# Performance work log

Measured on AMD Instinct MI355X. Metric: run time of the kernel, lower is better.

Reference implementation:

```python
import jax, jax.numpy as jnp
import numpy as np

SLOPE = 0.1
HEADS = 4
BN_EPS = 1e-5


def _gat(x, W, a_src, a_dst, mask):
    # x: (B,N,D); W: (D,D); a_src/a_dst: (H,dh); mask: (B,N,N) bool
    B, N, D = x.shape
    dh = D // HEADS
    h = (x @ W).reshape(B, N, HEADS, dh)
    s_src = jnp.einsum('bnhd,hd->bhn', h, a_src)  # score contrib of query i
    s_dst = jnp.einsum('bnhd,hd->bhn', h, a_dst)  # score contrib of key j
    e = jax.nn.leaky_relu(s_src[:, :, :, None] + s_dst[:, :, None, :], SLOPE)  # (B,H,N,N)
    e = jnp.where(mask[:, None, :, :], e, jnp.float32(-1e9))
    a = jax.nn.softmax(e, axis=-1)
    out = jnp.einsum('bhij,bjhd->bihd', a, h).reshape(B, N, D)
    return out


def setup_inputs() -> dict:
    key = jax.random.key(0)
    ks = jax.random.split(key, 20)
    B, N, F, D, Hn = 2, 2000, 64, 128, 3
    deep_dim = 3 * D
    feats = jax.random.normal(ks[0], (B, N, F), dtype=jnp.float32)
    ind = jax.random.randint(ks[1], (B, N, N), 0, 2).astype(bool)
    eye = jnp.eye(N, dtype=bool)[None]
    ind = jnp.logical_or(ind, eye)  # ensure self-loops so no all-masked row
    uni = jnp.ones((B, N, N), dtype=bool)
    s = 0.05
    return {
        'features': feats,
        'industry_mask': ind,
        'universe_mask': uni,
        # BatchNorm1d (eval mode)
        'bn_gamma': jax.random.normal(ks[2], (F,)) * s + 1.0,
        'bn_beta': jax.random.normal(ks[3], (F,)) * s,
        'bn_mean': jnp.zeros((F,), jnp.float32),
        'bn_var': jnp.ones((F,), jnp.float32),
        # encoder MLP (stored as (in,out))
        'W1': jax.random.normal(ks[4], (F, D)) * s,
        'b1': jnp.zeros((D,), jnp.float32),
        'W2': jax.random.normal(ks[5], (D, D)) * s,
        'b2': jnp.zeros((D,), jnp.float32),
        # industry GAT
        'giW': jax.random.normal(ks[6], (D, D)) * s,
        'gia_src': jax.random.normal(ks[7], (HEADS, D // HEADS)) * s,
        'gia_dst': jax.random.normal(ks[8], (HEADS, D // HEADS)) * s,
        # universe GAT
        'guW': jax.random.normal(ks[9], (D, D)) * s,
        'gua_src': jax.random.normal(ks[10], (HEADS, D // HEADS)) * s,
        'gua_dst': jax.random.normal(ks[11], (HEADS, D // HEADS)) * s,
        # per-horizon deep factor heads (Hn, deep_dim), (Hn,)
        'head_W': jax.random.normal(ks[12], (Hn, deep_dim)) * s,
        'head_b': jnp.zeros((Hn,), jnp.float32),
        # per-horizon factor attention proj (Hn, F, F), applied as x @ P_h^T
        'proj_W': jax.random.normal(ks[13], (Hn, F, F)) * s,
    }


def reference(features, industry_mask, universe_mask, bn_gamma, bn_beta, bn_mean,
              bn_var, W1, b1, W2, b2, giW, gia_src, gia_dst, guW, gua_src,
              gua_dst, head_W, head_b, proj_W):
    # --- StockContextEncoder: BN (eval) + MLP ---
    xn = (features - bn_mean) * jax.lax.rsqrt(bn_var + BN_EPS) * bn_gamma + bn_beta
    C = jax.nn.relu(xn @ W1 + b1) @ W2 + b2  # (B,N,D)
    # --- masked GATs with residual subtraction ---
    H_I = _gat(C, giW, gia_src, gia_dst, industry_mask)
    C_bar_I = C - H_I
    H_U = _gat(C_bar_I, guW, gua_src, gua_dst, universe_mask)
    C_bar_U = C_bar_I - H_U
    concat_ctx = jnp.concatenate([C, C_bar_I, C_bar_U], axis=-1)  # (B,N,3D)
    # --- per-horizon deep factor heads (vectorized over horizons) ---
    factors = jax.nn.leaky_relu(
        jnp.einsum('bnd,hd->hbn', concat_ctx, head_W) + head_b[:, None, None], SLOPE)
    # --- FactorAttention (Eq. 9-12), vectorized over horizons ---
    U = jax.nn.leaky_relu(jnp.einsum('bnm,hkm->hbnk', features, proj_W), SLOPE)
    A = jax.nn.softmax(U, axis=-1)          # (Hn,B,N,m)
    a_bar = A.mean(axis=2)                  # (Hn,B,m)
    recon = jnp.einsum('bnm,hbm->hbn', features, a_bar)
    return (C, C_bar_I, C_bar_U, H_I, H_U, factors, recon, A)
```

## Files before the change

### kernel.cpp

```cpp
#include <hip/hip_runtime.h>

#define BB 2
#define NN 2000
#define FF 64
#define DD 128
#define NH 4
#define HNZ 3
#define DEEP 384
#define NSEG 8
#define SEGSTRIDE 256
#define HTPAD 2048

typedef __attribute__((ext_vector_type(8))) short short8;
typedef __attribute__((ext_vector_type(4))) float f32x4;
typedef unsigned short ushort_t;

__device__ __forceinline__ float lrelu(float x) { return x > 0.f ? x : 0.1f * x; }
__device__ __forceinline__ ushort_t f2bf(float f) {
    unsigned int u = __float_as_uint(f);
    unsigned int r = u + 0x7fffu + ((u >> 16) & 1u);
    return (ushort_t)(r >> 16);
}

__global__ __launch_bounds__(128) void k_enc_proj(
    const float* __restrict__ feat, const float* __restrict__ gamma,
    const float* __restrict__ beta, const float* __restrict__ mean,
    const float* __restrict__ var, const float* __restrict__ W1,
    const float* __restrict__ b1, const float* __restrict__ W2,
    const float* __restrict__ b2, float* __restrict__ C,
    const float* __restrict__ Wg, const float* __restrict__ a_src,
    const float* __restrict__ a_dst, ushort_t* __restrict__ hb_rm,
    float* __restrict__ ssrc, float* __restrict__ sdst)
{
    __shared__ float xnl[4][FF];
    __shared__ float hidl[4][DD];
    __shared__ float Cl[4][DD];
    const int row0 = blockIdx.x * 4;
    const int t = threadIdx.x;
    for (int idx = t; idx < 4 * FF; idx += 128) {
        int r = idx >> 6, m = idx & 63;
        float f = feat[(row0 + r) * FF + m];
        xnl[r][m] = (f - mean[m]) * rsqrtf(var[m] + 1e-5f) * gamma[m] + beta[m];
    }
    __syncthreads();
    float acc[4];
    const int j = t;
#pragma unroll
    for (int r = 0; r < 4; ++r) acc[r] = b1[j];
    for (int m = 0; m < FF; ++m) {
        float w = W1[m * DD + j];
#pragma unroll
        for (int r = 0; r < 4; ++r) acc[r] += xnl[r][m] * w;
    }
#pragma unroll
    for (int r = 0; r < 4; ++r) hidl[r][j] = fmaxf(acc[r], 0.f);
    __syncthreads();
#pragma unroll
    for (int r = 0; r < 4; ++r) acc[r] = b2[j];
    for (int k = 0; k < DD; ++k) {
        float w = W2[k * DD + j];
#pragma unroll
        for (int r = 0; r < 4; ++r) acc[r] += hidl[r][k] * w;
    }
#pragma unroll
    for (int r = 0; r < 4; ++r) {
        C[(row0 + r) * DD + j] = acc[r];
        Cl[r][j] = acc[r];
    }
    __syncthreads();
    float pacc[4] = {0.f, 0.f, 0.f, 0.f};
    for (int k = 0; k < DD; ++k) {
        float w = Wg[k * DD + j];
#pragma unroll
        for (int r = 0; r < 4; ++r) pacc[r] += Cl[r][k] * w;
    }
    const float as = a_src[j], ad = a_dst[j];
    const int head = j >> 5;
#pragma unroll
    for (int r = 0; r < 4; ++r) {
        hb_rm[(row0 + r) * DD + j] = f2bf(pacc[r]);
        float ps = pacc[r] * as;
        float pd = pacc[r] * ad;
#pragma unroll
        for (int off = 16; off; off >>= 1) {
            ps += __shfl_xor(ps, off, 32);
            pd += __shfl_xor(pd, off, 32);
        }
        if ((j & 31) == 0) {
            int row = row0 + r;
            int b = row / NN, n = row % NN;
            ssrc[(b * NH + head) * NN + n] = ps;
            sdst[(b * NH + head) * NN + n] = pd;
        }
    }
}

__global__ __launch_bounds__(128) void k_finish_proj(
    const float* __restrict__ C, const float* __restrict__ den,
    float* __restrict__ H, float* __restrict__ Cbar,
    const float* __restrict__ Wg, const float* __restrict__ a_src,
    const float* __restrict__ a_dst, ushort_t* __restrict__ hb_rm,
    float* __restrict__ ssrc, float* __restrict__ sdst)
{
    __shared__ float Xl[4][DD];
    const int row0 = blockIdx.x * 4;
    const int t = threadIdx.x;
    const int hh = t >> 5;
#pragma unroll
    for (int r = 0; r < 4; ++r) {
        int idx = (row0 + r) * DD + t;
        float dv = den[(row0 + r) * NH + hh];
        float Hv = H[idx] / dv;
        float cb = C[idx] - Hv;
        H[idx] = Hv;
        Cbar[idx] = cb;
        Xl[r][t] = cb;
    }
    __syncthreads();
    float pacc[4] = {0.f, 0.f, 0.f, 0.f};
    const int j = t;
    for (int k = 0; k < DD; ++k) {
        float w = Wg[k * DD + j];
#pragma unroll
        for (int r = 0; r < 4; ++r) pacc[r] += Xl[r][k] * w;
    }
    const float as = a_src[j], ad = a_dst[j];
    const int head = j >> 5;
#pragma unroll
    for (int r = 0; r < 4; ++r) {
        hb_rm[(row0 + r) * DD + j] = f2bf(pacc[r]);
        float ps = pacc[r] * as;
        float pd = pacc[r] * ad;
#pragma unroll
        for (int off = 16; off; off >>= 1) {
            ps += __shfl_xor(ps, off, 32);
            pd += __shfl_xor(pd, off, 32);
        }
        if ((j & 31) == 0) {
            int row = row0 + r;
            int b = row / NN, n = row % NN;
            ssrc[(b * NH + head) * NN + n] = ps;
            sdst[(b * NH + head) * NN + n] = pd;
        }
    }
}

__global__ __launch_bounds__(256) void k_transpose(
    const ushort_t* __restrict__ hb_rm, ushort_t* __restrict__ hT)
{
    __shared__ ushort_t tile[64][65];
    const int nblk = blockIdx.x & 31;
    const int dblk = (blockIdx.x >> 5) & 1;
    const int b = blockIdx.x >> 6;
    const int n0 = nblk * 64, d0 = dblk * 64;
    const int t = threadIdx.x;
#pragma unroll
    for (int e = 0; e < 16; ++e) {
        int lin = e * 256 + t;
        int n = lin >> 6, d = lin & 63;
        if (n0 + n < NN)
            tile[n][d] = hb_rm[(b * NN + n0 + n) * DD + d0 + d];
    }
    __syncthreads();
#pragma unroll
    for (int e = 0; e < 16; ++e) {
        int lin = e * 256 + t;
        int d = lin >> 6, n = lin & 63;
        if (n0 + n < NN)
            hT[(b * DD + d0 + d) * HTPAD + n0 + n] = tile[n][d];
    }
}

__global__ __launch_bounds__(256) void k_gat_attn(
    const int* __restrict__ mask, const ushort_t* __restrict__ hT,
    const float* __restrict__ ssrc, const float* __restrict__ sdst,
    float* __restrict__ Hnum, float* __restrict__ den_out)
{
    __shared__ float sdl[NH][SEGSTRIDE];
    const int t = threadIdx.x;
    const int iblk = blockIdx.x % 125;
    const int tmp = blockIdx.x / 125;
    const int b = tmp & 1;
    const int seg = tmp >> 1;
    const int i0 = iblk * 16;
    const int jbeg = seg * SEGSTRIDE;
    const int jlim = min(NN - jbeg, SEGSTRIDE);

    const int h = t >> 6;
    const int l = t & 63;
    const int il = l & 15;
    const int g = l >> 4;

    for (int jj = l; jj < jlim; jj += 64)
        sdl[h][jj] = sdst[(b * NH + h) * NN + jbeg + jj];
    __syncthreads();

    const float sS = ssrc[(b * NH + h) * NN + i0 + il];
    const int* mrow = mask + (long)b * NN * NN + (long)(i0 + il) * NN + jbeg;
    const ushort_t* hrow0 = hT + ((b * DD + 32 * h + il) * HTPAD + jbeg);
    const ushort_t* hrow1 = hrow0 + 16 * HTPAD;

    f32x4 acc0 = {0.f, 0.f, 0.f, 0.f};
    f32x4 acc1 = {0.f, 0.f, 0.f, 0.f};
    float den_acc = 0.f;

    for (int jc = 0; jc < SEGSTRIDE; jc += 32) {
        const int jloc = jc + 8 * g;
        int4 m0 = make_int4(0, 0, 0, 0), m1 = make_int4(0, 0, 0, 0);
        if (jloc < jlim)     m0 = *(const int4*)(mrow + jloc);
        if (jloc + 4 < jlim) m1 = *(const int4*)(mrow + jloc + 4);
        float4 s0 = *(const float4*)&sdl[h][jloc];
        float4 s1 = *(const float4*)&sdl[h][jloc + 4];
        float w[8];
        w[0] = m0.x ? __expf(lrelu(sS + s0.x)) : 0.f;
        w[1] = m0.y ? __expf(lrelu(sS + s0.y)) : 0.f;
        w[2] = m0.z ? __expf(lrelu(sS + s0.z)) : 0.f;
        w[3] = m0.w ? __expf(lrelu(sS + s0.w)) : 0.f;
        w[4] = m1.x ? __expf(lrelu(sS + s1.x)) : 0.f;
        w[5] = m1.y ? __expf(lrelu(sS + s1.y)) : 0.f;
        w[6] = m1.z ? __expf(lrelu(sS + s1.z)) : 0.f;
        w[7] = m1.w ? __expf(lrelu(sS + s1.w)) : 0.f;
        short8 af;
#pragma unroll
        for (int e = 0; e < 8; ++e) {
            den_acc += w[e];
            af[e] = (short)f2bf(w[e]);
        }
        short8 bf0 = *(const short8*)(hrow0 + jloc);
        short8 bf1 = *(const short8*)(hrow1 + jloc);
        acc0 = __builtin_amdgcn_mfma_f32_16x16x32_bf16(af, bf0, acc0, 0, 0, 0);
        acc1 = __builtin_amdgcn_mfma_f32_16x16x32_bf16(af, bf1, acc1, 0, 0, 0);
    }

    den_acc += __shfl_xor(den_acc, 16);
    den_acc += __shfl_xor(den_acc, 32);
    if (l < 16)
        atomicAdd(&den_out[(b * NN + i0 + l) * NH + h], den_acc);

#pragma unroll
    for (int r = 0; r < 4; ++r) {
        float* dst = &Hnum[((long)b * NN + i0 + 4 * g + r) * DD + 32 * h + il];
        atomicAdd(dst, acc0[r]);
        atomicAdd(dst + 16, acc1[r]);
    }
}

__global__ __launch_bounds__(256) void k_finish(
    const float* __restrict__ X, const float* __restrict__ den,
    float* __restrict__ H, float* __restrict__ Cbar)
{
    int idx = blockIdx.x * 256 + threadIdx.x;
    if (idx >= BB * NN * DD / 4) return;
    int row = idx >> 5;
    int d4 = idx & 31;
    float inv = 1.f / den[row * NH + (d4 >> 3)];
    float4 s = ((const float4*)H)[idx];
    float4 xv = ((const float4*)X)[idx];
    float4 ho = make_float4(s.x * inv, s.y * inv, s.z * inv, s.w * inv);
    ((float4*)H)[idx] = ho;
    ((float4*)Cbar)[idx] =
        make_float4(xv.x - ho.x, xv.y - ho.y, xv.z - ho.z, xv.w - ho.w);
}

__global__ __launch_bounds__(256) void k_factors(
    const float* __restrict__ C, const float* __restrict__ CbI,
    const float* __restrict__ CbU, const float* __restrict__ head_W,
    const float* __restrict__ head_b, float* __restrict__ factors)
{
    int out = blockIdx.x * 4 + (threadIdx.x >> 6);
    int l = threadIdx.x & 63;
    if (out >= HNZ * BB * NN) return;
    int h = out / (BB * NN);
    int rn = out % (BB * NN);
    const float* w = head_W + h * DEEP;
    float acc = C[rn * DD + l] * w[l] + C[rn * DD + l + 64] * w[l + 64]
              + CbI[rn * DD + l] * w[128 + l] + CbI[rn * DD + l + 64] * w[192 + l]
              + CbU[rn * DD + l] * w[256 + l] + CbU[rn * DD + l + 64] * w[320 + l];
#pragma unroll
    for (int off = 32; off; off >>= 1) acc += __shfl_xor(acc, off, 64);
    if (l == 0) factors[out] = lrelu(acc + head_b[h]);
}

__global__ __launch_bounds__(256) void k_factor_attn(
    const float* __restrict__ feat, const float* __restrict__ proj_W,
    float* __restrict__ A, float* __restrict__ abar)
{
    __shared__ float Pt[FF][FF + 1];
    __shared__ float fl[4][FF];
    __shared__ float abpart[4][FF];
    const int hb = blockIdx.x / 50;
    const int n_base = (blockIdx.x % 50) * 40;
    const int h = hb / BB, b = hb % BB;
    const int t = threadIdx.x;
    for (int idx = t; idx < FF * FF; idx += 256) {
        int k = idx >> 6, m = idx & 63;
        Pt[m][k] = proj_W[(h * FF + k) * FF + m];
    }
    const int ns = t >> 6, k = t & 63;
    float abp = 0.f;
    for (int cch = 0; cch < 10; ++cch) {
        int n0 = n_base + cch * 4;
        __syncthreads();
        for (int idx = t; idx < 4 * FF; idx += 256) {
            int r = idx >> 6, m = idx & 63;
            fl[r][m] = feat[(b * NN + n0 + r) * FF + m];
        }
        __syncthreads();
        float u = 0.f;
        for (int m = 0; m < FF; ++m) u += fl[ns][m] * Pt[m][k];
        u = lrelu(u);
        float mx = u;
#pragma unroll
        for (int off = 32; off; off >>= 1) mx = fmaxf(mx, __shfl_xor(mx, off, 64));
        float e = __expf(u - mx);
        float sm = e;
#pragma unroll
        for (int off = 32; off; off >>= 1) sm += __shfl_xor(sm, off, 64);
        float a = e / sm;
        A[((h * BB + b) * NN + n0 + ns) * FF + k] = a;
        abp += a;
    }
    abpart[ns][k] = abp;
    __syncthreads();
    if (t < FF) {
        float s = abpart[0][t] + abpart[1][t] + abpart[2][t] + abpart[3][t];
        atomicAdd(&abar[(h * BB + b) * FF + t], s);
    }
}

__global__ __launch_bounds__(256) void k_recon(
    const float* __restrict__ feat, const float* __restrict__ abar,
    float* __restrict__ recon)
{
    int out = blockIdx.x * 4 + (threadIdx.x >> 6);
    int l = threadIdx.x & 63;
    if (out >= HNZ * BB * NN) return;
    int h = out / (BB * NN);
    int rn = out % (BB * NN);
    float acc = feat[rn * FF + l] * abar[(h * BB + rn / NN) * FF + l];
#pragma unroll
    for (int off = 32; off; off >>= 1) acc += __shfl_xor(acc, off, 64);
    if (l == 0) recon[out] = acc * (1.f / NN);
}

extern "C" void kernel_launch(void* const* d_in, const int* in_sizes, int n_in,
                              void* d_out, int out_size, void* d_ws, size_t ws_size,
                              hipStream_t stream)
{
    const float* feat     = (const float*)d_in[0];
    const int*   ind_mask = (const int*)d_in[1];
    const int*   uni_mask = (const int*)d_in[2];
    const float* bn_gamma = (const float*)d_in[3];
    const float* bn_beta  = (const float*)d_in[4];
    const float* bn_mean  = (const float*)d_in[5];
    const float* bn_var   = (const float*)d_in[6];
    const float* W1 = (const float*)d_in[7];
    const float* b1 = (const float*)d_in[8];
    const float* W2 = (const float*)d_in[9];
    const float* b2 = (const float*)d_in[10];
    const float* giW = (const float*)d_in[11];
    const float* gia_src = (const float*)d_in[12];
    const float* gia_dst = (const float*)d_in[13];
    const float* guW = (const float*)d_in[14];
    const float* gua_src = (const float*)d_in[15];
    const float* gua_dst = (const float*)d_in[16];
    const float* head_W = (const float*)d_in[17];
    const float* head_b = (const float*)d_in[18];
    const float* proj_W = (const float*)d_in[19];

    float* out = (float*)d_out;
    float* C       = out;
    float* CbI     = out + 512000;
    float* CbU     = out + 1024000;
    float* H_I     = out + 1536000;
    float* H_U     = out + 2048000;
    float* factors = out + 2560000;
    float* recon   = out + 2572000;
    float* A       = out + 2584000;

    float* ws = (float*)d_ws;
    ushort_t* hb_rm = (ushort_t*)ws;
    ushort_t* hT    = (ushort_t*)(ws + 256000);
    float* ssrc = ws + 518144;
    float* sdst = ws + 534144;
    float* den1 = ws + 550144;
    float* den2 = ws + 566144;
    float* abar = ws + 582144;

    hipMemsetAsync(H_I, 0, 1024000 * sizeof(float), stream);
    hipMemsetAsync(den1, 0, 32384 * sizeof(float), stream);

    k_enc_proj<<<BB * NN / 4, 128, 0, stream>>>(
        feat, bn_gamma, bn_beta, bn_mean, bn_var, W1, b1, W2, b2, C,
        giW, gia_src, gia_dst, hb_rm, ssrc, sdst);
    k_transpose<<<BB * 2 * 32, 256, 0, stream>>>(hb_rm, hT);
    k_gat_attn<<<NSEG * BB * 125, 256, 0, stream>>>(
        ind_mask, hT, ssrc, sdst, H_I, den1);
    k_finish_proj<<<BB * NN / 4, 128, 0, stream>>>(
        C, den1, H_I, CbI, guW, gua_src, gua_dst, hb_rm, ssrc, sdst);
    k_transpose<<<BB * 2 * 32, 256, 0, stream>>>(hb_rm, hT);
    k_gat_attn<<<NSEG * BB * 125, 256, 0, stream>>>(
        uni_mask, hT, ssrc, sdst, H_U, den2);
    k_finish<<<500, 256, 0, stream>>>(CbI, den2, H_U, CbU);

    k_factors<<<3000, 256, 0, stream>>>(C, CbI, CbU, head_W, head_b, factors);
    k_factor_attn<<<HNZ * BB * 50, 256, 0, stream>>>(feat, proj_W, A, abar);
    k_recon<<<3000, 256, 0, stream>>>(feat, abar, recon);
}
```

Before: 267.9 us.

## Fuse transpose into projection, replace atomics with per-segment partials, merge tail kernels

The projection kernels now write the transposed bf16 h directly, so the separate transpose kernels go away, and they process 16 rows per block with float4 register tiling. The GAT attention kernel uses 4 segments of 512 keys and writes per-segment partial numerators and denominators, which removes the atomics and the large memsets. The finish kernels sum those partials. Factor-attention is retiled to 8 rows per block and launched first, and the factors and recon kernels are merged into one. The cost is extra partial-buffer traffic in place of atomic contention.

```diff
diff --git a/kernel.cpp b/kernel.cpp
--- a/kernel.cpp
+++ b/kernel.cpp
@@ -7,13 +7,16 @@
 #define NH 4
 #define HNZ 3
 #define DEEP 384
-#define NSEG 8
-#define SEGSTRIDE 256
+#define NSEG 4
+#define SEGSTRIDE 512
 #define HTPAD 2048
+#define SEGTOT (BB * NN * DD)
+#define DENTOT (BB * NN * NH)
 
 typedef __attribute__((ext_vector_type(8))) short short8;
 typedef __attribute__((ext_vector_type(4))) float f32x4;
 typedef unsigned short ushort_t;
+typedef unsigned int uint_t;
 
 __device__ __forceinline__ float lrelu(float x) { return x > 0.f ? x : 0.1f * x; }
 __device__ __forceinline__ ushort_t f2bf(float f) {
@@ -22,159 +25,169 @@
     return (ushort_t)(r >> 16);
 }
 
-__global__ __launch_bounds__(128) void k_enc_proj(
+__device__ __forceinline__ void proj_scores(
+    const float (*Xl)[DD], const float* __restrict__ Wg,
+    const float* __restrict__ a_src, const float* __restrict__ a_dst,
+    ushort_t* __restrict__ hT, float* __restrict__ ssrc,
+    float* __restrict__ sdst, int row0, int t)
+{
+    const int jq = t & 31, rg = t >> 5;
+    const int r0 = 2 * rg, c0 = 4 * jq;
+    float4 p0 = make_float4(0.f, 0.f, 0.f, 0.f);
+    float4 p1 = make_float4(0.f, 0.f, 0.f, 0.f);
+    for (int k = 0; k < DD; ++k) {
+        float4 w = *(const float4*)&Wg[k * DD + c0];
+        float x0 = Xl[r0][k], x1 = Xl[r0 + 1][k];
+        p0.x += x0 * w.x; p0.y += x0 * w.y; p0.z += x0 * w.z; p0.w += x0 * w.w;
+        p1.x += x1 * w.x; p1.y += x1 * w.y; p1.z += x1 * w.z; p1.w += x1 * w.w;
+    }
+    const int gr = row0 + r0;
+    const int b = gr / NN, n = gr % NN;
+    uint_t pk;
+    pk = (uint_t)f2bf(p0.x) | ((uint_t)f2bf(p1.x) << 16);
+    *(uint_t*)&hT[(b * DD + c0 + 0) * HTPAD + n] = pk;
+    pk = (uint_t)f2bf(p0.y) | ((uint_t)f2bf(p1.y) << 16);
+    *(uint_t*)&hT[(b * DD + c0 + 1) * HTPAD + n] = pk;
+    pk = (uint_t)f2bf(p0.z) | ((uint_t)f2bf(p1.z) << 16);
+    *(uint_t*)&hT[(b * DD + c0 + 2) * HTPAD + n] = pk;
+    pk = (uint_t)f2bf(p0.w) | ((uint_t)f2bf(p1.w) << 16);
+    *(uint_t*)&hT[(b * DD + c0 + 3) * HTPAD + n] = pk;
+
+    float4 as4 = *(const float4*)&a_src[c0];
+    float4 ad4 = *(const float4*)&a_dst[c0];
+    float ps0 = p0.x * as4.x + p0.y * as4.y + p0.z * as4.z + p0.w * as4.w;
+    float ps1 = p1.x * as4.x + p1.y * as4.y + p1.z * as4.z + p1.w * as4.w;
+    float pd0 = p0.x * ad4.x + p0.y * ad4.y + p0.z * ad4.z + p0.w * ad4.w;
+    float pd1 = p1.x * ad4.x + p1.y * ad4.y + p1.z * ad4.z + p1.w * ad4.w;
+#pragma unroll
+    for (int off = 1; off <= 4; off <<= 1) {
+        ps0 += __shfl_xor(ps0, off);
+        ps1 += __shfl_xor(ps1, off);
+        pd0 += __shfl_xor(pd0, off);
+        pd1 += __shfl_xor(pd1, off);
+    }
+    if ((jq & 7) == 0) {
+        int h = jq >> 3;
+        ssrc[(b * NH + h) * NN + n] = ps0;
+        ssrc[(b * NH + h) * NN + n + 1] = ps1;
+        sdst[(b * NH + h) * NN + n] = pd0;
+        sdst[(b * NH + h) * NN + n + 1] = pd1;
+    }
+}
+
+__global__ __launch_bounds__(256) void k_enc_proj(
     const float* __restrict__ feat, const float* __restrict__ gamma,
     const float* __restrict__ beta, const float* __restrict__ mean,
     const float* __restrict__ var, const float* __restrict__ W1,
     const float* __restrict__ b1, const float* __restrict__ W2,
     const float* __restrict__ b2, float* __restrict__ C,
     const float* __restrict__ Wg, const float* __restrict__ a_src,
-    const float* __restrict__ a_dst, ushort_t* __restrict__ hb_rm,
+    const float* __restrict__ a_dst, ushort_t* __restrict__ hT,
     float* __restrict__ ssrc, float* __restrict__ sdst)
 {
-    __shared__ float xnl[4][FF];
-    __shared__ float hidl[4][DD];
-    __shared__ float Cl[4][DD];
-    const int row0 = blockIdx.x * 4;
+    __shared__ float xnl[16][FF];
+    __shared__ float hidl[16][DD];
+    __shared__ float Cl[16][DD];
+    const int row0 = blockIdx.x * 16;
     const int t = threadIdx.x;
-    for (int idx = t; idx < 4 * FF; idx += 128) {
-        int r = idx >> 6, m = idx & 63;
-        float f = feat[(row0 + r) * FF + m];
-        xnl[r][m] = (f - mean[m]) * rsqrtf(var[m] + 1e-5f) * gamma[m] + beta[m];
-    }
-    __syncthreads();
-    float acc[4];
-    const int j = t;
-#pragma unroll
-    for (int r = 0; r < 4; ++r) acc[r] = b1[j];
-    for (int m = 0; m < FF; ++m) {
-        float w = W1[m * DD + j];
-#pragma unroll
-        for (int r = 0; r < 4; ++r) acc[r] += xnl[r][m] * w;
-    }
-#pragma unroll
-    for (int r = 0; r < 4; ++r) hidl[r][j] = fmaxf(acc[r], 0.f);
-    __syncthreads();
-#pragma unroll
-    for (int r = 0; r < 4; ++r) acc[r] = b2[j];
+    {
+        int row = t >> 4, m0 = (t & 15) * 4;
+        float4 f = *(const float4*)&feat[(row0 + row) * FF + m0];
+        float4 g4 = *(const float4*)&gamma[m0];
+        float4 be4 = *(const float4*)&beta[m0];
+        float4 mn4 = *(const float4*)&mean[m0];
+        float4 vr4 = *(const float4*)&var[m0];
+        float4 xv;
+        xv.x = (f.x - mn4.x) * rsqrtf(vr4.x + 1e-5f) * g4.x + be4.x;
+        xv.y = (f.y - mn4.y) * rsqrtf(vr4.y + 1e-5f) * g4.y + be4.y;
+        xv.z = (f.z - mn4.z) * rsqrtf(vr4.z + 1e-5f) * g4.z + be4.z;
+        xv.w = (f.w - mn4.w) * rsqrtf(vr4.w + 1e-5f) * g4.w + be4.w;
+        *(float4*)&xnl[row][m0] = xv;
+    }
+    __syncthreads();
+    const int jq = t & 31, rg = t >> 5;
+    const int r0 = 2 * rg, c0 = 4 * jq;
+    float4 bb = *(const float4*)&b1[c0];
+    float4 a0 = bb, a1 = bb;
+    for (int k = 0; k < FF; ++k) {
+        float4 w = *(const float4*)&W1[k * DD + c0];
+        float x0 = xnl[r0][k], x1 = xnl[r0 + 1][k];
+        a0.x += x0 * w.x; a0.y += x0 * w.y; a0.z += x0 * w.z; a0.w += x0 * w.w;
+        a1.x += x1 * w.x; a1.y += x1 * w.y; a1.z += x1 * w.z; a1.w += x1 * w.w;
+    }
+    a0.x = fmaxf(a0.x, 0.f); a0.y = fmaxf(a0.y, 0.f);
+    a0.z = fmaxf(a0.z, 0.f); a0.w = fmaxf(a0.w, 0.f);
+    a1.x = fmaxf(a1.x, 0.f); a1.y = fmaxf(a1.y, 0.f);
+    a1.z = fmaxf(a1.z, 0.f); a1.w = fmaxf(a1.w, 0.f);
+    *(float4*)&hidl[r0][c0] = a0;
+    *(float4*)&hidl[r0 + 1][c0] = a1;
+    __syncthreads();
+    bb = *(const float4*)&b2[c0];
+    a0 = bb; a1 = bb;
     for (int k = 0; k < DD; ++k) {
-        float w = W2[k * DD + j];
-#pragma unroll
-        for (int r = 0; r < 4; ++r) acc[r] += hidl[r][k] * w;
-    }
-#pragma unroll
-    for (int r = 0; r < 4; ++r) {
-        C[(row0 + r) * DD + j] = acc[r];
-        Cl[r][j] = acc[r];
-    }
-    __syncthreads();
-    float pacc[4] = {0.f, 0.f, 0.f, 0.f};
-    for (int k = 0; k < DD; ++k) {
-        float w = Wg[k * DD + j];
-#pragma unroll
-        for (int r = 0; r < 4; ++r) pacc[r] += Cl[r][k] * w;
-    }
-    const float as = a_src[j], ad = a_dst[j];
-    const int head = j >> 5;
-#pragma unroll
-    for (int r = 0; r < 4; ++r) {
-        hb_rm[(row0 + r) * DD + j] = f2bf(pacc[r]);
-        float ps = pacc[r] * as;
-        float pd = pacc[r] * ad;
-#pragma unroll
-        for (int off = 16; off; off >>= 1) {
-            ps += __shfl_xor(ps, off, 32);
-            pd += __shfl_xor(pd, off, 32);
+        float4 w = *(const float4*)&W2[k * DD + c0];
+        float x0 = hidl[r0][k], x1 = hidl[r0 + 1][k];
+        a0.x += x0 * w.x; a0.y += x0 * w.y; a0.z += x0 * w.z; a0.w += x0 * w.w;
+        a1.x += x1 * w.x; a1.y += x1 * w.y; a1.z += x1 * w.z; a1.w += x1 * w.w;
+    }
+    *(float4*)&C[(row0 + r0) * DD + c0] = a0;
+    *(float4*)&C[(row0 + r0 + 1) * DD + c0] = a1;
+    *(float4*)&Cl[r0][c0] = a0;
+    *(float4*)&Cl[r0 + 1][c0] = a1;
+    __syncthreads();
+    proj_scores(Cl, Wg, a_src, a_dst, hT, ssrc, sdst, row0, t);
+}
+
+__global__ __launch_bounds__(256) void k_finish_proj(
+    const float* __restrict__ C, const float* __restrict__ num_p,
+    const float* __restrict__ den_p, float* __restrict__ H,
+    float* __restrict__ Cbar, const float* __restrict__ Wg,
+    const float* __restrict__ a_src, const float* __restrict__ a_dst,
+    ushort_t* __restrict__ hT, float* __restrict__ ssrc,
+    float* __restrict__ sdst)
+{
+    __shared__ float Xl[16][DD];
+    __shared__ float denl[16][NH];
+    const int row0 = blockIdx.x * 16;
+    const int t = threadIdx.x;
+    if (t < 64) {
+        int rr = t >> 2, hh = t & 3;
+        int gr = row0 + rr;
+        float s = 0.f;
+#pragma unroll
+        for (int sg = 0; sg < NSEG; ++sg)
+            s += den_p[sg * DENTOT + gr * NH + hh];
+        denl[rr][hh] = s;
+    }
+    __syncthreads();
+    const int jq = t & 31, rg = t >> 5;
+    const int r0 = 2 * rg, c0 = 4 * jq;
+    const int hh = jq >> 3;
+#pragma unroll
+    for (int rr = 0; rr < 2; ++rr) {
+        int gr = row0 + r0 + rr;
+        float4 s = make_float4(0.f, 0.f, 0.f, 0.f);
+#pragma unroll
+        for (int sg = 0; sg < NSEG; ++sg) {
+            float4 v = *(const float4*)&num_p[sg * SEGTOT + gr * DD + c0];
+            s.x += v.x; s.y += v.y; s.z += v.z; s.w += v.w;
         }
-        if ((j & 31) == 0) {
-            int row = row0 + r;
-            int b = row / NN, n = row % NN;
-            ssrc[(b * NH + head) * NN + n] = ps;
-            sdst[(b * NH + head) * NN + n] = pd;
-        }
-    }
-}
-
-__global__ __launch_bounds__(128) void k_finish_proj(
-    const float* __restrict__ C, const float* __restrict__ den,
-    float* __restrict__ H, float* __restrict__ Cbar,
-    const float* __restrict__ Wg, const float* __restrict__ a_src,
-    const float* __restrict__ a_dst, ushort_t* __restrict__ hb_rm,
-    float* __restrict__ ssrc, float* __restrict__ sdst)
-{
-    __shared__ float Xl[4][DD];
-    const int row0 = blockIdx.x * 4;
-    const int t = threadIdx.x;
-    const int hh = t >> 5;
-#pragma unroll
-    for (int r = 0; r < 4; ++r) {
-        int idx = (row0 + r) * DD + t;
-        float dv = den[(row0 + r) * NH + hh];
-        float Hv = H[idx] / dv;
-        float cb = C[idx] - Hv;
-        H[idx] = Hv;
-        Cbar[idx] = cb;
-        Xl[r][t] = cb;
-    }
-    __syncthreads();
-    float pacc[4] = {0.f, 0.f, 0.f, 0.f};
-    const int j = t;
-    for (int k = 0; k < DD; ++k) {
-        float w = Wg[k * DD + j];
-#pragma unroll
-        for (int r = 0; r < 4; ++r) pacc[r] += Xl[r][k] * w;
-    }
-    const float as = a_src[j], ad = a_dst[j];
-    const int head = j >> 5;
-#pragma unroll
-    for (int r = 0; r < 4; ++r) {
-        hb_rm[(row0 + r) * DD + j] = f2bf(pacc[r]);
-        float ps = pacc[r] * as;
-        float pd = pacc[r] * ad;
-#pragma unroll
-        for (int off = 16; off; off >>= 1) {
-            ps += __shfl_xor(ps, off, 32);
-            pd += __shfl_xor(pd, off, 32);
-        }
-        if ((j & 31) == 0) {
-            int row = row0 + r;
-            int b = row / NN, n = row % NN;
-            ssrc[(b * NH + head) * NN + n] = ps;
-            sdst[(b * NH + head) * NN + n] = pd;
-        }
-    }
-}
-
-__global__ __launch_bounds__(256) void k_transpose(
-    const ushort_t* __restrict__ hb_rm, ushort_t* __restrict__ hT)
-{
-    __shared__ ushort_t tile[64][65];
-    const int nblk = blockIdx.x & 31;
-    const int dblk = (blockIdx.x >> 5) & 1;
-    const int b = blockIdx.x >> 6;
-    const int n0 = nblk * 64, d0 = dblk * 64;
-    const int t = threadIdx.x;
-#pragma unroll
-    for (int e = 0; e < 16; ++e) {
-        int lin = e * 256 + t;
-        int n = lin >> 6, d = lin & 63;
-        if (n0 + n < NN)
-            tile[n][d] = hb_rm[(b * NN + n0 + n) * DD + d0 + d];
-    }
-    __syncthreads();
-#pragma unroll
-    for (int e = 0; e < 16; ++e) {
-        int lin = e * 256 + t;
-        int d = lin >> 6, n = lin & 63;
-        if (n0 + n < NN)
-            hT[(b * DD + d0 + d) * HTPAD + n0 + n] = tile[n][d];
-    }
+        float inv = 1.f / denl[r0 + rr][hh];
+        float4 cv = *(const float4*)&C[gr * DD + c0];
+        float4 Hv = make_float4(s.x * inv, s.y * inv, s.z * inv, s.w * inv);
+        float4 cb = make_float4(cv.x - Hv.x, cv.y - Hv.y, cv.z - Hv.z, cv.w - Hv.w);
+        *(float4*)&H[gr * DD + c0] = Hv;
+        *(float4*)&Cbar[gr * DD + c0] = cb;
+        *(float4*)&Xl[r0 + rr][c0] = cb;
+    }
+    __syncthreads();
+    proj_scores(Xl, Wg, a_src, a_dst, hT, ssrc, sdst, row0, t);
 }
 
 __global__ __launch_bounds__(256) void k_gat_attn(
     const int* __restrict__ mask, const ushort_t* __restrict__ hT,
     const float* __restrict__ ssrc, const float* __restrict__ sdst,
-    float* __restrict__ Hnum, float* __restrict__ den_out)
+    float* __restrict__ num_p, float* __restrict__ den_p)
 {
     __shared__ float sdl[NH][SEGSTRIDE];
     const int t = threadIdx.x;
@@ -235,26 +248,37 @@
     den_acc += __shfl_xor(den_acc, 16);
     den_acc += __shfl_xor(den_acc, 32);
     if (l < 16)
-        atomicAdd(&den_out[(b * NN + i0 + l) * NH + h], den_acc);
-
+        den_p[seg * DENTOT + (b * NN + i0 + l) * NH + h] = den_acc;
+
+    const long segbase = (long)seg * SEGTOT;
 #pragma unroll
     for (int r = 0; r < 4; ++r) {
-        float* dst = &Hnum[((long)b * NN + i0 + 4 * g + r) * DD + 32 * h + il];
-        atomicAdd(dst, acc0[r]);
-        atomicAdd(dst + 16, acc1[r]);
+        long base = segbase + ((long)b * NN + i0 + 4 * g + r) * DD + 32 * h + il;
+        num_p[base] = acc0[r];
+        num_p[base + 16] = acc1[r];
     }
 }
 
 __global__ __launch_bounds__(256) void k_finish(
-    const float* __restrict__ X, const float* __restrict__ den,
-    float* __restrict__ H, float* __restrict__ Cbar)
+    const float* __restrict__ X, const float* __restrict__ num_p,
+    const float* __restrict__ den_p, float* __restrict__ H,
+    float* __restrict__ Cbar)
 {
     int idx = blockIdx.x * 256 + threadIdx.x;
     if (idx >= BB * NN * DD / 4) return;
     int row = idx >> 5;
     int d4 = idx & 31;
-    float inv = 1.f / den[row * NH + (d4 >> 3)];
-    float4 s = ((const float4*)H)[idx];
+    float den = 0.f;
+#pragma unroll
+    for (int sg = 0; sg < NSEG; ++sg)
+        den += den_p[sg * DENTOT + row * NH + (d4 >> 3)];
+    float4 s = make_float4(0.f, 0.f, 0.f, 0.f);
+#pragma unroll
+    for (int sg = 0; sg < NSEG; ++sg) {
+        float4 v = ((const float4*)(num_p + (long)sg * SEGTOT))[idx];
+        s.x += v.x; s.y += v.y; s.z += v.z; s.w += v.w;
+    }
+    float inv = 1.f / den;
     float4 xv = ((const float4*)X)[idx];
     float4 ho = make_float4(s.x * inv, s.y * inv, s.z * inv, s.w * inv);
     ((float4*)H)[idx] = ho;
@@ -262,10 +286,65 @@
         make_float4(xv.x - ho.x, xv.y - ho.y, xv.z - ho.z, xv.w - ho.w);
 }
 
-__global__ __launch_bounds__(256) void k_factors(
+__global__ __launch_bounds__(256) void k_factor_attn(
+    const float* __restrict__ feat, const float* __restrict__ proj_W,
+    float* __restrict__ A, float* __restrict__ abar)
+{
+    __shared__ float Pt[FF][FF + 1];
+    __shared__ float fl[8][FF];
+    __shared__ float abpart[4][FF];
+    const int hb = blockIdx.x / 250;
+    const int n_base = (blockIdx.x % 250) * 8;
+    const int h = hb >> 1, b = hb & 1;
+    const int t = threadIdx.x;
+    for (int idx = t; idx < FF * FF; idx += 256) {
+        int k = idx >> 6, m = idx & 63;
+        Pt[m][k] = proj_W[(h * FF + k) * FF + m];
+    }
+    for (int idx = t; idx < 8 * FF / 4; idx += 256) {
+        int r = idx >> 4, m0 = (idx & 15) * 4;
+        *(float4*)&fl[r][m0] =
+            *(const float4*)&feat[(b * NN + n_base + r) * FF + m0];
+    }
+    __syncthreads();
+    const int ns = t >> 6, k = t & 63;
+    float u0 = 0.f, u1 = 0.f;
+    for (int m = 0; m < FF; ++m) {
+        float p = Pt[m][k];
+        u0 += fl[ns][m] * p;
+        u1 += fl[ns + 4][m] * p;
+    }
+    u0 = lrelu(u0); u1 = lrelu(u1);
+    float mx0 = u0, mx1 = u1;
+#pragma unroll
+    for (int off = 32; off; off >>= 1) {
+        mx0 = fmaxf(mx0, __shfl_xor(mx0, off));
+        mx1 = fmaxf(mx1, __shfl_xor(mx1, off));
+    }
+    float e0 = __expf(u0 - mx0), e1 = __expf(u1 - mx1);
+    float sm0 = e0, sm1 = e1;
+#pragma unroll
+    for (int off = 32; off; off >>= 1) {
+        sm0 += __shfl_xor(sm0, off);
+        sm1 += __shfl_xor(sm1, off);
+    }
+    float a0 = e0 / sm0, a1 = e1 / sm1;
+    A[((h * BB + b) * NN + n_base + ns) * FF + k] = a0;
+    A[((h * BB + b) * NN + n_base + ns + 4) * FF + k] = a1;
+    abpart[ns][k] = a0 + a1;
+    __syncthreads();
+    if (t < FF) {
+        float s = abpart[0][t] + abpart[1][t] + abpart[2][t] + abpart[3][t];
+        atomicAdd(&abar[(h * BB + b) * FF + t], s);
+    }
+}
+
+__global__ __launch_bounds__(256) void k_factors_recon(
     const float* __restrict__ C, const float* __restrict__ CbI,
     const float* __restrict__ CbU, const float* __restrict__ head_W,
-    const float* __restrict__ head_b, float* __restrict__ factors)
+    const float* __restrict__ head_b, const float* __restrict__ feat,
+    const float* __restrict__ abar, float* __restrict__ factors,
+    float* __restrict__ recon)
 {
     int out = blockIdx.x * 4 + (threadIdx.x >> 6);
     int l = threadIdx.x & 63;
@@ -276,71 +355,16 @@
     float acc = C[rn * DD + l] * w[l] + C[rn * DD + l + 64] * w[l + 64]
               + CbI[rn * DD + l] * w[128 + l] + CbI[rn * DD + l + 64] * w[192 + l]
               + CbU[rn * DD + l] * w[256 + l] + CbU[rn * DD + l + 64] * w[320 + l];
-#pragma unroll
-    for (int off = 32; off; off >>= 1) acc += __shfl_xor(acc, off, 64);
-    if (l == 0) factors[out] = lrelu(acc + head_b[h]);
-}
-
-__global__ __launch_bounds__(256) void k_factor_attn(
-    const float* __restrict__ feat, const float* __restrict__ proj_W,
-    float* __restrict__ A, float* __restrict__ abar)
-{
-    __shared__ float Pt[FF][FF + 1];
-    __shared__ float fl[4][FF];
-    __shared__ float abpart[4][FF];
-    const int hb = blockIdx.x / 50;
-    const int n_base = (blockIdx.x % 50) * 40;
-    const int h = hb / BB, b = hb % BB;
-    const int t = threadIdx.x;
-    for (int idx = t; idx < FF * FF; idx += 256) {
-        int k = idx >> 6, m = idx & 63;
-        Pt[m][k] = proj_W[(h * FF + k) * FF + m];
-    }
-    const int ns = t >> 6, k = t & 63;
-    float abp = 0.f;
-    for (int cch = 0; cch < 10; ++cch) {
-        int n0 = n_base + cch * 4;
-        __syncthreads();
-        for (int idx = t; idx < 4 * FF; idx += 256) {
-            int r = idx >> 6, m = idx & 63;
-            fl[r][m] = feat[(b * NN + n0 + r) * FF + m];
-        }
-        __syncthreads();
-        float u = 0.f;
-        for (int m = 0; m < FF; ++m) u += fl[ns][m] * Pt[m][k];
-        u = lrelu(u);
-        float mx = u;
-#pragma unroll
-        for (int off = 32; off; off >>= 1) mx = fmaxf(mx, __shfl_xor(mx, off, 64));
-        float e = __expf(u - mx);
-        float sm = e;
-#pragma unroll
-        for (int off = 32; off; off >>= 1) sm += __shfl_xor(sm, off, 64);
-        float a = e / sm;
-        A[((h * BB + b) * NN + n0 + ns) * FF + k] = a;
-        abp += a;
-    }
-    abpart[ns][k] = abp;
-    __syncthreads();
-    if (t < FF) {
-        float s = abpart[0][t] + abpart[1][t] + abpart[2][t] + abpart[3][t];
-        atomicAdd(&abar[(h * BB + b) * FF + t], s);
-    }
-}
-
-__global__ __launch_bounds__(256) void k_recon(
-    const float* __restrict__ feat, const float* __restrict__ abar,
-    float* __restrict__ recon)
-{
-    int out = blockIdx.x * 4 + (threadIdx.x >> 6);
-    int l = threadIdx.x & 63;
-    if (out >= HNZ * BB * NN) return;
-    int h = out / (BB * NN);
-    int rn = out % (BB * NN);
-    float acc = feat[rn * FF + l] * abar[(h * BB + rn / NN) * FF + l];
-#pragma unroll
-    for (int off = 32; off; off >>= 1) acc += __shfl_xor(acc, off, 64);
-    if (l == 0) recon[out] = acc * (1.f / NN);
+    float racc = feat[rn * FF + l] * abar[(h * BB + rn / NN) * FF + l];
+#pragma unroll
+    for (int off = 32; off; off >>= 1) {
+        acc += __shfl_xor(acc, off);
+        racc += __shfl_xor(racc, off);
+    }
+    if (l == 0) {
+        factors[out] = lrelu(acc + head_b[h]);
+        recon[out] = racc * (1.f / NN);
+    }
 }
 
 extern "C" void kernel_launch(void* const* d_in, const int* in_sizes, int n_in,
@@ -379,31 +403,28 @@
     float* A       = out + 2584000;
 
     float* ws = (float*)d_ws;
-    ushort_t* hb_rm = (ushort_t*)ws;
-    ushort_t* hT    = (ushort_t*)(ws + 256000);
-    float* ssrc = ws + 518144;
-    float* sdst = ws + 534144;
-    float* den1 = ws + 550144;
-    float* den2 = ws + 566144;
-    float* abar = ws + 582144;
-
-    hipMemsetAsync(H_I, 0, 1024000 * sizeof(float), stream);
-    hipMemsetAsync(den1, 0, 32384 * sizeof(float), stream);
-
-    k_enc_proj<<<BB * NN / 4, 128, 0, stream>>>(
+    ushort_t* hT = (ushort_t*)ws;
+    float* ssrc  = ws + 262400;
+    float* sdst  = ws + 278400;
+    float* den_p = ws + 294400;
+    float* num_p = ws + 358400;
+    float* abar  = ws + 2406400;
+
+    hipMemsetAsync(abar, 0, HNZ * BB * FF * sizeof(float), stream);
+
+    k_factor_attn<<<HNZ * BB * 250, 256, 0, stream>>>(feat, proj_W, A, abar);
+
+    k_enc_proj<<<BB * NN / 16, 256, 0, stream>>>(
         feat, bn_gamma, bn_beta, bn_mean, bn_var, W1, b1, W2, b2, C,
-        giW, gia_src, gia_dst, hb_rm, ssrc, sdst);
-    k_transpose<<<BB * 2 * 32, 256, 0, stream>>>(hb_rm, hT);
+        giW, gia_src, gia_dst, hT, ssrc, sdst);
     k_gat_attn<<<NSEG * BB * 125, 256, 0, stream>>>(
-        ind_mask, hT, ssrc, sdst, H_I, den1);
-    k_finish_proj<<<BB * NN / 4, 128, 0, stream>>>(
-        C, den1, H_I, CbI, guW, gua_src, gua_dst, hb_rm, ssrc, sdst);
-    k_transpose<<<BB * 2 * 32, 256, 0, stream>>>(hb_rm, hT);
+        ind_mask, hT, ssrc, sdst, num_p, den_p);
+    k_finish_proj<<<BB * NN / 16, 256, 0, stream>>>(
+        C, num_p, den_p, H_I, CbI, guW, gua_src, gua_dst, hT, ssrc, sdst);
     k_gat_attn<<<NSEG * BB * 125, 256, 0, stream>>>(
-        uni_mask, hT, ssrc, sdst, H_U, den2);
-    k_finish<<<500, 256, 0, stream>>>(CbI, den2, H_U, CbU);
-
-    k_factors<<<3000, 256, 0, stream>>>(C, CbI, CbU, head_W, head_b, factors);
-    k_factor_attn<<<HNZ * BB * 50, 256, 0, stream>>>(feat, proj_W, A, abar);
-    k_recon<<<3000, 256, 0, stream>>>(feat, abar, recon);
-}
+        uni_mask, hT, ssrc, sdst, num_p, den_p);
+    k_finish<<<500, 256, 0, stream>>>(CbI, num_p, den_p, H_U, CbU);
+
+    k_factors_recon<<<3000, 256, 0, stream>>>(
+        C, CbI, CbU, head_W, head_b, feat, abar, factors, recon);
+}
```

Result: faster. 239.2 us (-10.7%).
